# Performance work log

Measured on AMD Instinct MI355X. Metric: run time of the kernel, lower is better.

Reference implementation:

```python
import jax, jax.numpy as jnp
import numpy as np
import math

E, K = 8, 4
IN, OUT = 768, 768
B, S = 16, 512

def _nearest_factors(n):
    r = int(math.sqrt(n))
    while n % r != 0:
        r -= 1
    r = max(r, 1)
    return r, n // r

D1, D2 = _nearest_factors(IN)      # 24, 32
DO1, DO2 = _nearest_factors(OUT)   # 24, 32

def _cv_squared(v):
    v = v.astype(jnp.float32)
    return jnp.var(v, ddof=1) / (jnp.mean(v) ** 2 + 1e-10)

def setup_inputs() -> dict:
    key = jax.random.key(0)
    ks = jax.random.split(key, 8)
    eye = lambda d: jnp.broadcast_to(jnp.eye(d, dtype=jnp.float32), (E, d, d))
    return {
        "x": jax.random.normal(ks[0], (B, S, IN), jnp.float32),
        "w_gate": 0.02 * jax.random.normal(ks[1], (IN, E), jnp.float32),
        "weight": 0.02 * jax.random.normal(ks[2], (E, OUT, IN), jnp.float32),
        "res_weight": 0.02 * jax.random.normal(ks[3], (OUT, IN), jnp.float32),
        "curve1_in": eye(D1) + 0.01 * jax.random.normal(ks[4], (E, D1, D1), jnp.float32),
        "curve2_in": eye(D2) + 0.01 * jax.random.normal(ks[5], (E, D2, D2), jnp.float32),
        "curve1_out": eye(DO1) + 0.01 * jax.random.normal(ks[6], (E, DO1, DO1), jnp.float32),
        "curve2_out": eye(DO2) + 0.01 * jax.random.normal(ks[7], (E, DO2, DO2), jnp.float32),
    }

def reference(x, w_gate, weight, res_weight, curve1_in, curve2_in, curve1_out, curve2_out):
    b = x.shape[0]
    # ---- noisy_top_k_gating (eval mode: clean logits, no noise) ----
    xm = x.mean(-2)                         # [B, IN]
    logits = xm @ w_gate                    # [B, E]
    top_vals, top_idx = jax.lax.top_k(logits, min(K + 1, E))
    tk_vals = top_vals[:, :K]
    tk_idx = top_idx[:, :K]
    tk_gates = jax.nn.softmax(tk_vals, axis=1)
    gates = jnp.zeros_like(logits).at[jnp.arange(b)[:, None], tk_idx].set(tk_gates)
    load = (gates > 0).sum(0)               # eval: gates_to_load
    importance = gates.sum(0)
    loss = 0.01 * (_cv_squared(importance) + _cv_squared(load))
    # ---- curve-factor expert weight composition (k*2 >= n_experts branch) ----
    rtw = (weight - res_weight).reshape(E, DO1, DO2, D1, D2)
    rtw = jnp.einsum('bij,bjklm->biklm', curve1_out, rtw)
    rtw = jnp.einsum('bik,bjklm->bjilm', curve2_out, rtw)
    rtw = jnp.einsum('bil,bjklm->bjkim', curve1_in, rtw)
    rtw = jnp.einsum('bim,bjklm->bjkli', curve2_in, rtw)
    rtw = rtw.reshape(E, OUT, IN)
    # dropout p=0.1 is identity in eval mode
    expert_weights = res_weight + 0.9 * jnp.sum(rtw[None] * gates[:, :, None, None], axis=1)  # [B, OUT, IN]
    y = jnp.einsum('bsj,bkj->bsk', x, expert_weights)  # [B, S, OUT]
    return y, loss
```

## Files before the change

### kernel.cpp

```cpp
#include <hip/hip_runtime.h>
#include <hip/hip_bf16.h>

typedef unsigned short u16;
typedef __attribute__((ext_vector_type(8))) short bf16x8;
typedef __attribute__((ext_vector_type(4))) float f32x4;

#define NE 8
#define NTOPK 4
#define NIN 768
#define NOUT 768
#define NB 16
#define NS 512
#define YSZ (NB * NS * NOUT)
#define EWN (NOUT * NIN)

#define OFF_PART  0u
#define OFF_GATES 3145728u
#define OFF_XBF   3146240u
#define OFF_WD    15729152u
#define OFF_T1T   25166336u
#define OFF_RTW   34603520u
#define OFF_EW    44040704u

#define PRE_BAR(N) asm volatile("s_waitcnt vmcnt(" #N ")\n\ts_barrier" ::: "memory")
#define POST_BAR() asm volatile("s_waitcnt lgkmcnt(0)\n\ts_barrier" ::: "memory")

__device__ __forceinline__ u16 f2bf(float f) {
  union { float f; unsigned u; } v; v.f = f;
  unsigned r = v.u + 0x7fffu + ((v.u >> 16) & 1u);
  return (u16)(r >> 16);
}
__device__ __forceinline__ float bf2f(u16 h) {
  union { unsigned u; float f; } v; v.u = ((unsigned)h) << 16;
  return v.f;
}
__device__ __forceinline__ unsigned cvt2(float a, float b) {
  unsigned r;
  asm("v_cvt_pk_bf16_f32 %0, %1, %2" : "=v"(r) : "v"(a), "v"(b));
  return r;
}
__device__ __forceinline__ void gload16(const void* g, void* l) {
  __builtin_amdgcn_global_load_lds(
      (const __attribute__((address_space(1))) unsigned int*)g,
      (__attribute__((address_space(3))) unsigned int*)l, 16, 0, 0);
}
__device__ __forceinline__ void storeC(float* p, float v) { *p = v; }
__device__ __forceinline__ void storeC(u16* p, float v) { *p = f2bf(v); }

__global__ __launch_bounds__(256) void k_wd(const float* __restrict__ w,
                                            const float* __restrict__ res,
                                            u16* __restrict__ Wd) {
  int b2 = blockIdx.x;
  int e = b2 / 288;
  int blk = b2 % 288;
  size_t base = (size_t)blk * 2048 + threadIdx.x * 8;
  float4 wa = *(const float4*)(w + (size_t)e * EWN + base);
  float4 wb = *(const float4*)(w + (size_t)e * EWN + base + 4);
  float4 ra = *(const float4*)(res + base);
  float4 rb = *(const float4*)(res + base + 4);
  bf16x8 o;
  o[0] = (short)f2bf(wa.x - ra.x); o[1] = (short)f2bf(wa.y - ra.y);
  o[2] = (short)f2bf(wa.z - ra.z); o[3] = (short)f2bf(wa.w - ra.w);
  o[4] = (short)f2bf(wb.x - rb.x); o[5] = (short)f2bf(wb.y - rb.y);
  o[6] = (short)f2bf(wb.z - rb.z); o[7] = (short)f2bf(wb.w - rb.w);
  *(bf16x8*)(Wd + (size_t)e * EWN + base) = o;
}

__device__ __forceinline__ void body_x(int u, const float* __restrict__ x,
                                       float* __restrict__ part,
                                       u16* __restrict__ xbf) {
  int t = threadIdx.x;
  if (t < 192) {
    int b = u >> 6;
    int sc = u & 63;
    int c = t * 4;
    float a0 = 0.f, a1 = 0.f, a2 = 0.f, a3 = 0.f;
    int s0 = sc * 8;
#pragma unroll
    for (int r = 0; r < 8; ++r) {
      size_t ro = ((size_t)(b * NS + s0 + r)) * NIN;
      float4 v = *(const float4*)(x + ro + c);
      a0 += v.x; a1 += v.y; a2 += v.z; a3 += v.w;
      ushort4 o;
      o.x = f2bf(v.x); o.y = f2bf(v.y); o.z = f2bf(v.z); o.w = f2bf(v.w);
      *(ushort4*)(xbf + ro + c) = o;
    }
    float4 pv; pv.x = a0; pv.y = a1; pv.z = a2; pv.w = a3;
    *(float4*)(part + (size_t)(b * 64 + sc) * NIN + c) = pv;
  }
}

__device__ __forceinline__ void body_logits(int b, float* red,
                                            const float* __restrict__ part,
                                            const float* __restrict__ w_gate,
                                            float* __restrict__ gates_out) {
  int tid = threadIdx.x;
  float p[NE] = {0.f, 0.f, 0.f, 0.f, 0.f, 0.f, 0.f, 0.f};
  for (int i = tid; i < NIN; i += 256) {
    float s = 0.f;
#pragma unroll
    for (int sc = 0; sc < 64; ++sc) s += part[(size_t)(b * 64 + sc) * NIN + i];
    float xmv = s * (1.0f / (float)NS);
#pragma unroll
    for (int e = 0; e < NE; ++e) p[e] += xmv * w_gate[i * NE + e];
  }
#pragma unroll
  for (int e = 0; e < NE; ++e) {
    float v = p[e];
    for (int off = 32; off; off >>= 1) v += __shfl_down(v, off);
    if ((tid & 63) == 0) red[(tid >> 6) * NE + e] = v;
  }
  __syncthreads();
  if (tid == 0) {
    float v[NE]; bool used[NE];
    for (int e = 0; e < NE; ++e) {
      v[e] = red[e] + red[NE + e] + red[2 * NE + e] + red[3 * NE + e];
      used[e] = false;
    }
    int idxs[NTOPK]; float vals[NTOPK];
    for (int t = 0; t < NTOPK; ++t) {
      int best = 0; float bv = -3.4e38f;
      for (int e = 0; e < NE; ++e)
        if (!used[e] && v[e] > bv) { bv = v[e]; best = e; }
      used[best] = true; idxs[t] = best; vals[t] = bv;
    }
    float m = vals[0];
    float ex[NTOPK]; float se = 0.f;
    for (int t = 0; t < NTOPK; ++t) { ex[t] = expf(vals[t] - m); se += ex[t]; }
    float g[NE];
    for (int e = 0; e < NE; ++e) g[e] = 0.f;
    for (int t = 0; t < NTOPK; ++t) g[idxs[t]] = ex[t] / se;
    for (int e = 0; e < NE; ++e) gates_out[b * NE + e] = g[e];
  }
}

__device__ __forceinline__ void body_kron(int bid, u16* lb,
                                          const float* __restrict__ c1,
                                          const float* __restrict__ c2,
                                          const u16* __restrict__ B,
                                          u16* __restrict__ C) {
  const int tid = threadIdx.x;
  const int lane = tid & 63;
  const int w = tid >> 6;
  const int wr = w >> 1, wc = w & 1;
  const int fr = lane & 15;
  const int kq = lane >> 4;
  const int swz = (bid & 7) * 72 + (bid >> 3);
  const int mb = swz % 12;
  const int nb = (swz / 12) % 6;
  const int e = swz / 72;
  const int m0 = mb * 64, n0 = nb * 128;
  const u16* Bb = B + (size_t)e * EWN;
  const float* c1b = c1 + e * 24 * 24;
  const float* c2b = c2 + e * 32 * 32;
  const int r1a = (m0 >> 5) + wr;
  float c2r[2][8];
  {
    const float* p0 = c2b + fr * 32 + kq * 8;
    const float* p1 = c2b + (16 + fr) * 32 + kq * 8;
#pragma unroll
    for (int j = 0; j < 8; ++j) { c2r[0][j] = p0[j]; c2r[1][j] = p1[j]; }
  }
  const int ob1 = (w * 2) * 1024 + lane * 16;
  const int ob2 = ob1 + 1024;
  const int rowB1 = ob1 >> 6, colB1 = ob1 & 63;
  const int rowB2 = ob2 >> 6, colB2 = ob2 & 63;

  auto STAGE = [&](int t) {
    int s = t & 3;
    int k0 = t * 32;
    gload16((const char*)Bb + ((size_t)(n0 + rowB1) * NIN + k0) * 2 + colB1,
            (char*)(lb + s * 4096) + ob1);
    gload16((const char*)Bb + ((size_t)(n0 + rowB2) * NIN + k0) * 2 + colB2,
            (char*)(lb + s * 4096) + ob2);
  };
  f32x4 acc[2][4] = {};
  auto COMPUTE = [&](int t) {
    int s = t & 3;
    const float ca = c1b[r1a * 24 + t];
    bf16x8 aF[2], bF[4];
#pragma unroll
    for (int m = 0; m < 2; ++m) {
      const float* cr = c2r[m];
      union { unsigned u[4]; bf16x8 v; } pk;
      pk.u[0] = cvt2(ca * cr[0], ca * cr[1]);
      pk.u[1] = cvt2(ca * cr[2], ca * cr[3]);
      pk.u[2] = cvt2(ca * cr[4], ca * cr[5]);
      pk.u[3] = cvt2(ca * cr[6], ca * cr[7]);
      aF[m] = pk.v;
    }
#pragma unroll
    for (int n = 0; n < 4; ++n)
      bF[n] = *(const bf16x8*)(lb + (size_t)s * 4096 + (wc * 64 + n * 16 + fr) * 32 + kq * 8);
#pragma unroll
    for (int m = 0; m < 2; ++m)
#pragma unroll
      for (int n = 0; n < 4; ++n)
        acc[m][n] = __builtin_amdgcn_mfma_f32_16x16x32_bf16(aF[m], bF[n], acc[m][n], 0, 0, 0);
  };

  STAGE(0); STAGE(1); STAGE(2); STAGE(3);
  for (int i = 0; i < 10; ++i) {
    PRE_BAR(4);
    COMPUTE(2 * i); COMPUTE(2 * i + 1);
    POST_BAR();
    STAGE(2 * i + 4); STAGE(2 * i + 5);
  }
  PRE_BAR(4);  COMPUTE(20); COMPUTE(21);  POST_BAR();
  PRE_BAR(0);  COMPUTE(22); COMPUTE(23);

  u16* Cb = C + (size_t)e * EWN;
#pragma unroll
  for (int m = 0; m < 2; ++m) {
    int rb = m0 + wr * 32 + m * 16 + kq * 4;
#pragma unroll
    for (int n = 0; n < 4; ++n) {
      int col = n0 + wc * 64 + n * 16 + fr;
#pragma unroll
      for (int r = 0; r < 4; ++r)
        storeC(Cb + (size_t)(rb + r) * NIN + col, acc[m][n][r]);
    }
  }
}

__global__ __launch_bounds__(256) void k_A(const float* c1, const float* c2,
                                           const u16* B, u16* C,
                                           const float* __restrict__ x,
                                           float* __restrict__ part,
                                           u16* __restrict__ xbf) {
  __shared__ __attribute__((aligned(128))) u16 lB[4 * 128 * 32];
  if (blockIdx.x < 576) body_kron(blockIdx.x, lB, c1, c2, B, C);
  else                  body_x(blockIdx.x - 576, x, part, xbf);
}

__global__ __launch_bounds__(256) void k_B(const float* c1, const float* c2,
                                           const u16* B, u16* C,
                                           const float* part, const float* w_gate,
                                           float* gates) {
  __shared__ __attribute__((aligned(128))) u16 lB[4 * 128 * 32];
  __shared__ float red[NB * NE];
  if (blockIdx.x < 576) body_kron(blockIdx.x, lB, c1, c2, B, C);
  else                  body_logits(blockIdx.x - 576, red, part, w_gate, gates);
}

__global__ __launch_bounds__(256) void k_p3(const u16* __restrict__ rtwb,
                                            const float* __restrict__ res,
                                            const float* __restrict__ g,
                                            u16* __restrict__ ew,
                                            float* __restrict__ loss_out) {
  __shared__ float gsh[NB * NE];
  int bid = blockIdx.x;
  int tid = threadIdx.x;
  if (tid < NB * NE) gsh[tid] = 0.9f * g[tid];
  __syncthreads();
  if (bid == 0 && tid == 0) {
    float imp[NE], ld[NE];
    for (int e = 0; e < NE; ++e) {
      float si = 0.f, sl = 0.f;
      for (int b = 0; b < NB; ++b) {
        float gg = g[b * NE + e];
        si += gg; sl += (gg > 0.f) ? 1.f : 0.f;
      }
      imp[e] = si; ld[e] = sl;
    }
    float loss = 0.f;
    for (int which = 0; which < 2; ++which) {
      const float* a = which ? ld : imp;
      float mean = 0.f;
      for (int e = 0; e < NE; ++e) mean += a[e];
      mean *= (1.0f / NE);
      float var = 0.f;
      for (int e = 0; e < NE; ++e) { float d = a[e] - mean; var += d * d; }
      var *= (1.0f / (NE - 1));
      loss += var / (mean * mean + 1e-10f);
    }
    loss_out[0] = 0.01f * loss;
  }
  size_t base = ((size_t)bid * 256 + tid) * 8;
  float rv[NE][8];
#pragma unroll
  for (int e = 0; e < NE; ++e) {
    bf16x8 v = *(const bf16x8*)(rtwb + (size_t)e * EWN + base);
#pragma unroll
    for (int j = 0; j < 8; ++j) rv[e][j] = bf2f((u16)v[j]);
  }
  float r8[8];
  {
    float4 ra = *(const float4*)(res + base);
    float4 rb = *(const float4*)(res + base + 4);
    r8[0] = ra.x; r8[1] = ra.y; r8[2] = ra.z; r8[3] = ra.w;
    r8[4] = rb.x; r8[5] = rb.y; r8[6] = rb.z; r8[7] = rb.w;
  }
  for (int b = 0; b < NB; ++b) {
    float a[8];
#pragma unroll
    for (int j = 0; j < 8; ++j) a[j] = r8[j];
#pragma unroll
    for (int e = 0; e < NE; ++e) {
      float gg = gsh[b * NE + e];
#pragma unroll
      for (int j = 0; j < 8; ++j) a[j] += gg * rv[e][j];
    }
    bf16x8 o;
#pragma unroll
    for (int j = 0; j < 8; ++j) o[j] = (short)f2bf(a[j]);
    *(bf16x8*)(ew + (size_t)b * EWN + base) = o;
  }
}

__global__ __launch_bounds__(256) void k_main(const u16* __restrict__ A,
                                              const u16* __restrict__ Bw,
                                              float* __restrict__ C) {
  __shared__ __attribute__((aligned(128))) u16 la[3 * 128 * 32];
  __shared__ __attribute__((aligned(128))) u16 lb[3 * 128 * 32];
  const int tid = threadIdx.x;
  const int lane = tid & 63;
  const int w = tid >> 6;
  const int wr = w >> 1, wc = w & 1;
  const int fr = lane & 15;
  const int kq = lane >> 4;
  const int swz = (blockIdx.x & 7) * 48 + (blockIdx.x >> 3);
  const int mb = swz % 4;
  const int nb = (swz / 4) % 6;
  const int b = swz / 24;
  const int m0 = mb * 128, n0 = nb * 128;
  const u16* Ab = A + (size_t)b * NS * NIN;
  const u16* Bb = Bw + (size_t)b * EWN;
  const int ob1 = tid * 16;
  const int ob2 = ob1 + 4096;
  const int row1 = ob1 >> 6, col1 = ob1 & 63;
  const int row2 = ob2 >> 6, col2 = ob2 & 63;

  auto STAGE = [&](int t) {
    int s = t % 3;
    int k0 = t * 32;
    gload16((const char*)Ab + ((size_t)(m0 + row1) * NIN + k0) * 2 + col1,
            (char*)(la + s * 4096) + ob1);
    gload16((const char*)Ab + ((size_t)(m0 + row2) * NIN + k0) * 2 + col2,
            (char*)(la + s * 4096) + ob2);
    gload16((const char*)Bb + ((size_t)(n0 + row1) * NIN + k0) * 2 + col1,
            (char*)(lb + s * 4096) + ob1);
    gload16((const char*)Bb + ((size_t)(n0 + row2) * NIN + k0) * 2 + col2,
            (char*)(lb + s * 4096) + ob2);
  };
  f32x4 acc[4][4] = {};
  auto COMPUTE = [&](int t) {
    int s = t % 3;
    bf16x8 aF[4], bF[4];
#pragma unroll
    for (int m = 0; m < 4; ++m)
      aF[m] = *(const bf16x8*)(la + (size_t)s * 4096 + (wr * 64 + m * 16 + fr) * 32 + kq * 8);
#pragma unroll
    for (int n = 0; n < 4; ++n)
      bF[n] = *(const bf16x8*)(lb + (size_t)s * 4096 + (wc * 64 + n * 16 + fr) * 32 + kq * 8);
#pragma unroll
    for (int m = 0; m < 4; ++m)
#pragma unroll
      for (int n = 0; n < 4; ++n)
        acc[m][n] = __builtin_amdgcn_mfma_f32_16x16x32_bf16(aF[m], bF[n], acc[m][n], 0, 0, 0);
  };

  STAGE(0); STAGE(1); STAGE(2);
  for (int i = 0; i < 10; ++i) {
    PRE_BAR(4);
    COMPUTE(2 * i); COMPUTE(2 * i + 1);
    POST_BAR();
    STAGE(2 * i + 3); STAGE(2 * i + 4);
  }
  PRE_BAR(4);  COMPUTE(20); COMPUTE(21);  POST_BAR();
  STAGE(23);
  PRE_BAR(0);  COMPUTE(22); COMPUTE(23);

  float* Cb = C + (size_t)b * NS * NOUT;
#pragma unroll
  for (int m = 0; m < 4; ++m) {
    int rb = m0 + wr * 64 + m * 16 + kq * 4;
#pragma unroll
    for (int n = 0; n < 4; ++n) {
      int col = n0 + wc * 64 + n * 16 + fr;
#pragma unroll
      for (int r = 0; r < 4; ++r)
        Cb[(size_t)(rb + r) * NOUT + col] = acc[m][n][r];
    }
  }
}

extern "C" void kernel_launch(void* const* d_in, const int* in_sizes, int n_in,
                              void* d_out, int out_size, void* d_ws, size_t ws_size,
                              hipStream_t stream) {
  const float* x = (const float*)d_in[0];
  const float* w_gate = (const float*)d_in[1];
  const float* weight = (const float*)d_in[2];
  const float* res_w = (const float*)d_in[3];
  const float* c1i = (const float*)d_in[4];
  const float* c2i = (const float*)d_in[5];
  const float* c1o = (const float*)d_in[6];
  const float* c2o = (const float*)d_in[7];

  char* ws = (char*)d_ws;
  float* part = (float*)(ws + OFF_PART);
  float* gates = (float*)(ws + OFF_GATES);
  u16* xbf = (u16*)(ws + OFF_XBF);
  u16* Wd = (u16*)(ws + OFF_WD);
  u16* T1t = (u16*)(ws + OFF_T1T);
  u16* rtwb = (u16*)(ws + OFF_RTW);
  u16* ew = (u16*)(ws + OFF_EW);

  float* y = (float*)d_out;
  float* loss = y + YSZ;

  k_wd<<<dim3(2304), 256, 0, stream>>>(weight, res_w, Wd);
  k_A<<<dim3(1600), 256, 0, stream>>>(c1i, c2i, Wd, T1t, x, part, xbf);
  k_B<<<dim3(592), 256, 0, stream>>>(c1o, c2o, T1t, rtwb, part, w_gate, gates);
  k_p3<<<dim3(288), 256, 0, stream>>>(rtwb, res_w, gates, ew, loss);
  k_main<<<dim3(384), 256, 0, stream>>>(xbf, ew, y);
}
```

Measured before the change: 72.91 us.

## Halve GEMM M-tile to 64 and deepen LDS pipeline to four stages

The main batched GEMM tile changes from 128x128 to 64x128, doubling the grid from 384 to 768 workgroups so more of the CUs are busy. The LDS ring buffer grows from three to four stages, with prefetch and wait counts adjusted to match. In exchange, each block reuses less data, since the B tile is now reloaded once for every 64 rows of A, and each warp issues fewer MFMAs per LDS load.

```diff
diff --git a/kernel.cpp b/kernel.cpp
--- a/kernel.cpp
+++ b/kernel.cpp
@@ -311,70 +311,69 @@
 __global__ __launch_bounds__(256) void k_main(const u16* __restrict__ A,
                                               const u16* __restrict__ Bw,
                                               float* __restrict__ C) {
-  __shared__ __attribute__((aligned(128))) u16 la[3 * 128 * 32];
-  __shared__ __attribute__((aligned(128))) u16 lb[3 * 128 * 32];
+  __shared__ __attribute__((aligned(128))) u16 lA[4][64 * 32];
+  __shared__ __attribute__((aligned(128))) u16 lB[4][128 * 32];
   const int tid = threadIdx.x;
   const int lane = tid & 63;
   const int w = tid >> 6;
   const int wr = w >> 1, wc = w & 1;
   const int fr = lane & 15;
   const int kq = lane >> 4;
-  const int swz = (blockIdx.x & 7) * 48 + (blockIdx.x >> 3);
-  const int mb = swz % 4;
-  const int nb = (swz / 4) % 6;
-  const int b = swz / 24;
-  const int m0 = mb * 128, n0 = nb * 128;
+  const int swz = (blockIdx.x & 7) * 96 + (blockIdx.x >> 3);
+  const int mb = swz % 8;
+  const int nb = (swz / 8) % 6;
+  const int b = swz / 48;
+  const int m0 = mb * 64, n0 = nb * 128;
   const u16* Ab = A + (size_t)b * NS * NIN;
   const u16* Bb = Bw + (size_t)b * EWN;
-  const int ob1 = tid * 16;
-  const int ob2 = ob1 + 4096;
-  const int row1 = ob1 >> 6, col1 = ob1 & 63;
-  const int row2 = ob2 >> 6, col2 = ob2 & 63;
+  const int obA = tid * 16;
+  const int rowA = obA >> 6, colA = obA & 63;
+  const int obB1 = (w * 2) * 1024 + lane * 16;
+  const int obB2 = obB1 + 1024;
+  const int rowB1 = obB1 >> 6, colB1 = obB1 & 63;
+  const int rowB2 = obB2 >> 6, colB2 = obB2 & 63;
 
   auto STAGE = [&](int t) {
-    int s = t % 3;
+    int s = t & 3;
     int k0 = t * 32;
-    gload16((const char*)Ab + ((size_t)(m0 + row1) * NIN + k0) * 2 + col1,
-            (char*)(la + s * 4096) + ob1);
-    gload16((const char*)Ab + ((size_t)(m0 + row2) * NIN + k0) * 2 + col2,
-            (char*)(la + s * 4096) + ob2);
-    gload16((const char*)Bb + ((size_t)(n0 + row1) * NIN + k0) * 2 + col1,
-            (char*)(lb + s * 4096) + ob1);
-    gload16((const char*)Bb + ((size_t)(n0 + row2) * NIN + k0) * 2 + col2,
-            (char*)(lb + s * 4096) + ob2);
+    gload16((const char*)Ab + ((size_t)(m0 + rowA) * NIN + k0) * 2 + colA,
+            (char*)&lA[s][0] + obA);
+    gload16((const char*)Bb + ((size_t)(n0 + rowB1) * NIN + k0) * 2 + colB1,
+            (char*)&lB[s][0] + obB1);
+    gload16((const char*)Bb + ((size_t)(n0 + rowB2) * NIN + k0) * 2 + colB2,
+            (char*)&lB[s][0] + obB2);
   };
-  f32x4 acc[4][4] = {};
+  f32x4 acc[2][4] = {};
   auto COMPUTE = [&](int t) {
-    int s = t % 3;
-    bf16x8 aF[4], bF[4];
-#pragma unroll
-    for (int m = 0; m < 4; ++m)
-      aF[m] = *(const bf16x8*)(la + (size_t)s * 4096 + (wr * 64 + m * 16 + fr) * 32 + kq * 8);
+    int s = t & 3;
+    bf16x8 aF[2], bF[4];
+#pragma unroll
+    for (int m = 0; m < 2; ++m)
+      aF[m] = *(const bf16x8*)&lA[s][(wr * 32 + m * 16 + fr) * 32 + kq * 8];
 #pragma unroll
     for (int n = 0; n < 4; ++n)
-      bF[n] = *(const bf16x8*)(lb + (size_t)s * 4096 + (wc * 64 + n * 16 + fr) * 32 + kq * 8);
-#pragma unroll
-    for (int m = 0; m < 4; ++m)
+      bF[n] = *(const bf16x8*)&lB[s][(wc * 64 + n * 16 + fr) * 32 + kq * 8];
+#pragma unroll
+    for (int m = 0; m < 2; ++m)
 #pragma unroll
       for (int n = 0; n < 4; ++n)
         acc[m][n] = __builtin_amdgcn_mfma_f32_16x16x32_bf16(aF[m], bF[n], acc[m][n], 0, 0, 0);
   };
 
-  STAGE(0); STAGE(1); STAGE(2);
+  STAGE(0); STAGE(1); STAGE(2); STAGE(3);
   for (int i = 0; i < 10; ++i) {
-    PRE_BAR(4);
+    PRE_BAR(6);
     COMPUTE(2 * i); COMPUTE(2 * i + 1);
     POST_BAR();
-    STAGE(2 * i + 3); STAGE(2 * i + 4);
-  }
-  PRE_BAR(4);  COMPUTE(20); COMPUTE(21);  POST_BAR();
-  STAGE(23);
+    STAGE(2 * i + 4); STAGE(2 * i + 5);
+  }
+  PRE_BAR(6);  COMPUTE(20); COMPUTE(21);  POST_BAR();
   PRE_BAR(0);  COMPUTE(22); COMPUTE(23);
 
   float* Cb = C + (size_t)b * NS * NOUT;
 #pragma unroll
-  for (int m = 0; m < 4; ++m) {
-    int rb = m0 + wr * 64 + m * 16 + kq * 4;
+  for (int m = 0; m < 2; ++m) {
+    int rb = m0 + wr * 32 + m * 16 + kq * 4;
 #pragma unroll
     for (int n = 0; n < 4; ++n) {
       int col = n0 + wc * 64 + n * 16 + fr;
@@ -413,5 +412,5 @@
   k_A<<<dim3(1600), 256, 0, stream>>>(c1i, c2i, Wd, T1t, x, part, xbf);
   k_B<<<dim3(592), 256, 0, stream>>>(c1o, c2o, T1t, rtwb, part, w_gate, gates);
   k_p3<<<dim3(288), 256, 0, stream>>>(rtwb, res_w, gates, ew, loss);
-  k_main<<<dim3(384), 256, 0, stream>>>(xbf, ew, y);
-}
+  k_main<<<dim3(768), 256, 0, stream>>>(xbf, ew, y);
+}
```

New measurement: 73.96 us. No clear change (+1.4%).
